# Performance work log

Hardware: AMD Instinct MI355X
Metric: run time of the kernel (lower is better)

The kernel has to match this reference:

```python
import jax, jax.numpy as jnp
import numpy as np

B, M, L, LQ, E, V = 32, 100, 30, 30, 256, 32000


def position_encoding(seq_len, emb):
    # faithful to MemN2N position encoding: 1 + 4*(k - (E+1)/2)*(j - (J+1)/2)/(E*J)
    j = jnp.arange(1, seq_len + 1, dtype=jnp.float32)[:, None]   # (J,1)
    k = jnp.arange(1, emb + 1, dtype=jnp.float32)[None, :]       # (1,E)
    half_e = (emb + 1) / 2.0
    half_j = (seq_len + 1) / 2.0
    return 1.0 + 4.0 * (k - half_e) * (j - half_j) / (emb * seq_len)  # (J,E)


def masked_softmax(x, m):
    xm = jnp.where(m > 0, x, -1e30)
    e = jnp.exp(xm - jnp.max(xm, axis=-1, keepdims=True)) * m
    return e / (jnp.sum(e, axis=-1, keepdims=True) + 1e-13)


def masked_log_softmax(x, m):
    return jax.nn.log_softmax(x + jnp.log(m + 1e-13), axis=-1)


def _forward(trainS, trainQ, trainVM, trainPM, trainSM, trainQM,
             A1, A2, A3, A4, W, b, gamma, beta):
    # query encoding: embed + position encode + query mask + sum over words
    Q = trainQ[:, 0, :]                                   # (B,LQ)
    pe_q = position_encoding(LQ, E)                       # (LQ,E)
    u = jnp.sum(A1[Q] * pe_q * trainQM[:, :, None], axis=1)  # (B,E)

    # story memory embeddings: gather + PE + sum over words.
    # NOTE: original code multiplies by trainSM but discards the result (bug),
    # so SM is intentionally NOT applied here.
    pe_s = position_encoding(L, E)                        # (L,E)
    embA1 = jnp.sum(A1[trainS] * pe_s, axis=2)            # (B,M,E)
    embA2 = jnp.sum(A2[trainS] * pe_s, axis=2)
    embA3 = jnp.sum(A3[trainS] * pe_s, axis=2)
    embA4 = jnp.sum(A4[trainS] * pe_s, axis=2)

    def hop(memA, memC, u):
        # scores = sum_E(memA * u) * PM (PM applied pre-sum is equivalent)
        scores = jnp.einsum('bme,be->bm', memA, u) * trainPM
        p = masked_softmax(scores, trainPM)               # (B,M)
        o = jnp.einsum('bm,bme->be', p, memC)             # (B,E)
        return o + u

    u = hop(embA1, embA2, u)   # hop 1
    u = hop(embA2, embA3, u)   # hop 2
    u = hop(embA3, embA4, u)   # hop 3

    # final linear + BatchNorm1d (training-mode batch stats, eps=1e-5)
    wx = u @ W.T + b                                      # (B,V)
    mean = jnp.mean(wx, axis=0)
    var = jnp.mean((wx - mean) ** 2, axis=0)
    y = gamma * (wx - mean) / jnp.sqrt(var + 1e-5) + beta
    return masked_log_softmax(y, trainVM)


def setup_inputs() -> dict:
    key = jax.random.key(0)
    ks = jax.random.split(key, 8)
    inp = {
        'trainS': jax.random.randint(ks[0], (B, M, L), 0, V, dtype=jnp.int32),
        'trainQ': jax.random.randint(ks[1], (B, 1, LQ), 0, V, dtype=jnp.int32),
        'trainVM': jnp.ones((B, V), jnp.float32),
        'trainPM': jnp.ones((B, M), jnp.float32),
        'trainSM': jnp.ones((B, M, L), jnp.float32),
        'trainQM': jnp.ones((B, LQ), jnp.float32),
        'A1': 0.1 * jax.random.normal(ks[2], (V, E), jnp.float32),
        'A2': 0.1 * jax.random.normal(ks[3], (V, E), jnp.float32),
        'A3': 0.1 * jax.random.normal(ks[4], (V, E), jnp.float32),
        'A4': 0.1 * jax.random.normal(ks[5], (V, E), jnp.float32),
        'W': jax.random.normal(ks[6], (V, E), jnp.float32) / np.sqrt(E),
        'b': jnp.zeros((V,), jnp.float32),
        'gamma': jnp.ones((V,), jnp.float32),
        'beta': jnp.zeros((V,), jnp.float32),
        'inspect': 0,
    }
    return inp


def reference(trainS, trainQ, trainVM, trainPM, trainSM, trainQM,
              A1, A2, A3, A4, W, b, gamma, beta, inspect):
    return _forward(trainS, trainQ, trainVM, trainPM, trainSM, trainQM,
                    A1, A2, A3, A4, W, b, gamma, beta)
```

## Files before the change

### kernel.cpp

```cpp
#include <hip/hip_runtime.h>
#include <math.h>

static constexpr int B_ = 32, M_ = 100, L_ = 30, LQ_ = 30, E_ = 256, V_ = 32000;

__global__ __launch_bounds__(256) void k_embed(const int* __restrict__ trainS,
                                               const float* __restrict__ A1,
                                               const float* __restrict__ A2,
                                               const float* __restrict__ A3,
                                               const float* __restrict__ A4,
                                               float* __restrict__ embA) {
    const int bm = blockIdx.x;
    const int tbl = threadIdx.x >> 6;
    const int e0 = (threadIdx.x & 63) * 4;
    const float* __restrict__ A = (tbl == 0) ? A1 : (tbl == 1) ? A2 : (tbl == 2) ? A3 : A4;
    const float half_e = (E_ + 1) * 0.5f;
    const float half_j = (L_ + 1) * 0.5f;
    const float inv = 1.0f / (float)(E_ * L_);
    const float k0 = (float)(e0 + 1) - half_e;
    const float k1 = k0 + 1.f, k2 = k0 + 2.f, k3 = k0 + 3.f;

    int idx[L_];
#pragma unroll
    for (int l = 0; l < L_; ++l) idx[l] = trainS[bm * L_ + l];

    float4 acc = make_float4(0.f, 0.f, 0.f, 0.f);
#pragma unroll
    for (int c = 0; c < 2; ++c) {
        float4 r[15];
#pragma unroll
        for (int j = 0; j < 15; ++j)
            r[j] = *reinterpret_cast<const float4*>(A + (size_t)idx[c * 15 + j] * E_ + e0);
        __builtin_amdgcn_sched_barrier(0);
#pragma unroll
        for (int j = 0; j < 15; ++j) {
            const int l = c * 15 + j;
            const float coef = 4.0f * ((float)(l + 1) - half_j) * inv;
            acc.x += r[j].x * (1.0f + coef * k0);
            acc.y += r[j].y * (1.0f + coef * k1);
            acc.z += r[j].z * (1.0f + coef * k2);
            acc.w += r[j].w * (1.0f + coef * k3);
        }
    }
    *reinterpret_cast<float4*>(embA + (size_t)tbl * (B_ * M_ * E_) + (size_t)bm * E_ + e0) = acc;
}

__global__ __launch_bounds__(1024) void k_hops(const int* __restrict__ trainQ,
                                               const float* __restrict__ trainQM,
                                               const float* __restrict__ A1,
                                               const float* __restrict__ embA,
                                               const float* __restrict__ trainPM,
                                               float* __restrict__ u_T) {
    const int b = blockIdx.x;
    const int tid = threadIdx.x;
    const int lane = tid & 63;
    const int wave = tid >> 6;
    const int g = tid >> 8;
    const int e = tid & 255;
    __shared__ float u_sh[E_];
    __shared__ float sc[M_];
    __shared__ float p_sh[M_];
    __shared__ float osum[4][E_];

    {
        const float half_e = (E_ + 1) * 0.5f;
        const float half_j = (LQ_ + 1) * 0.5f;
        const float inv = 1.0f / (float)(E_ * LQ_);
        const float ke = (float)(e + 1) - half_e;
        const int l0 = g * 8;
        const int ln = (LQ_ - l0 < 8) ? (LQ_ - l0) : 8;
        int qi[8];
        float qm[8];
#pragma unroll
        for (int j = 0; j < 8; ++j) {
            if (j < ln) {
                qi[j] = trainQ[b * LQ_ + l0 + j];
                qm[j] = trainQM[b * LQ_ + l0 + j];
            } else { qi[j] = 0; qm[j] = 0.f; }
        }
        float r[8];
#pragma unroll
        for (int j = 0; j < 8; ++j)
            r[j] = (j < ln) ? A1[(size_t)qi[j] * E_ + e] : 0.f;
        float part = 0.f;
#pragma unroll
        for (int j = 0; j < 8; ++j) {
            const float pe = 1.0f + 4.0f * ke * ((float)(l0 + j + 1) - half_j) * inv;
            part += r[j] * pe * qm[j];
        }
        osum[g][e] = part;
    }
    __syncthreads();
    if (tid < E_) u_sh[tid] = osum[0][tid] + osum[1][tid] + osum[2][tid] + osum[3][tid];
    __syncthreads();

    for (int hop = 0; hop < 3; ++hop) {
        const float* memA = embA + (size_t)hop * (B_ * M_ * E_) + (size_t)b * M_ * E_;
        const float* memC = memA + (size_t)(B_ * M_ * E_);
#pragma unroll 2
        for (int m = wave; m < M_; m += 16) {
            const float* row = memA + m * E_;
            float part = 0.f;
#pragma unroll
            for (int j = 0; j < 4; ++j)
                part += row[lane + 64 * j] * u_sh[lane + 64 * j];
#pragma unroll
            for (int off = 32; off > 0; off >>= 1)
                part += __shfl_xor(part, off, 64);
            if (lane == 0) sc[m] = part * trainPM[b * M_ + m];
        }
        __syncthreads();
        if (wave == 0) {
            const float pm0 = (lane < M_) ? trainPM[b * M_ + lane] : 0.f;
            const float pm1 = (lane + 64 < M_) ? trainPM[b * M_ + lane + 64] : 0.f;
            const float x0 = (lane < M_ && pm0 > 0.f) ? sc[lane] : -1e30f;
            const float x1 = (lane + 64 < M_ && pm1 > 0.f) ? sc[lane + 64] : -1e30f;
            float mx = fmaxf(x0, x1);
#pragma unroll
            for (int off = 32; off > 0; off >>= 1)
                mx = fmaxf(mx, __shfl_xor(mx, off, 64));
            const float e0v = (lane < M_) ? expf(x0 - mx) * pm0 : 0.f;
            const float e1v = (lane + 64 < M_) ? expf(x1 - mx) * pm1 : 0.f;
            float ssum = e0v + e1v;
#pragma unroll
            for (int off = 32; off > 0; off >>= 1)
                ssum += __shfl_xor(ssum, off, 64);
            const float invs = 1.0f / (ssum + 1e-13f);
            if (lane < M_) p_sh[lane] = e0v * invs;
            if (lane + 64 < M_) p_sh[lane + 64] = e1v * invs;
        }
        __syncthreads();
        {
            float acc = 0.f;
            const float* crow = memC + e;
            const int m0 = g * 25;
#pragma unroll 5
            for (int mm = 0; mm < 25; ++mm)
                acc += p_sh[m0 + mm] * crow[(size_t)(m0 + mm) * E_];
            osum[g][e] = acc;
        }
        __syncthreads();
        if (tid < E_) u_sh[tid] += osum[0][tid] + osum[1][tid] + osum[2][tid] + osum[3][tid];
        __syncthreads();
    }
    if (tid < E_) u_T[tid * B_ + b] = u_sh[tid];
}

__global__ __launch_bounds__(256) void k_output(const float* __restrict__ u_T,
                                                const float* __restrict__ Wm,
                                                const float* __restrict__ bias,
                                                const float* __restrict__ gamma,
                                                const float* __restrict__ beta,
                                                const float* __restrict__ VM,
                                                float* __restrict__ z) {
    __shared__ float u_lds[E_ * B_];
    const int tid = threadIdx.x;
    for (int i = tid; i < (E_ * B_) / 4; i += 256)
        reinterpret_cast<float4*>(u_lds)[i] = reinterpret_cast<const float4*>(u_T)[i];
    __syncthreads();

    const int bg = tid & 7;
    const int vl = tid >> 3;
    const int v0 = blockIdx.x * 64 + vl * 2;
    const int v1 = v0 + 1;
    const float* __restrict__ wr0 = Wm + (size_t)v0 * E_;
    const float* __restrict__ wr1 = Wm + (size_t)v1 * E_;

    float accA[4] = {0.f, 0.f, 0.f, 0.f};
    float accB[4] = {0.f, 0.f, 0.f, 0.f};

#pragma unroll
    for (int c = 0; c < 8; ++c) {
        float4 wa[8], wb[8];
#pragma unroll
        for (int j = 0; j < 8; ++j) {
            wa[j] = reinterpret_cast<const float4*>(wr0)[c * 8 + j];
            wb[j] = reinterpret_cast<const float4*>(wr1)[c * 8 + j];
        }
        __builtin_amdgcn_sched_barrier(0);
#pragma unroll
        for (int j = 0; j < 8; ++j) {
#pragma unroll
            for (int eo = 0; eo < 4; ++eo) {
                const int e = c * 32 + j * 4 + eo;
                const float4 u4 = *reinterpret_cast<const float4*>(u_lds + e * B_ + bg * 4);
                const float w0 = (eo == 0) ? wa[j].x : (eo == 1) ? wa[j].y : (eo == 2) ? wa[j].z : wa[j].w;
                const float w1 = (eo == 0) ? wb[j].x : (eo == 1) ? wb[j].y : (eo == 2) ? wb[j].z : wb[j].w;
                accA[0] += w0 * u4.x; accA[1] += w0 * u4.y; accA[2] += w0 * u4.z; accA[3] += w0 * u4.w;
                accB[0] += w1 * u4.x; accB[1] += w1 * u4.y; accB[2] += w1 * u4.z; accB[3] += w1 * u4.w;
            }
        }
    }

    const float bvA = bias[v0], bvB = bias[v1];
    float s1a = 0.f, s2a = 0.f, s1b = 0.f, s2b = 0.f;
#pragma unroll
    for (int i = 0; i < 4; ++i) {
        accA[i] += bvA; accB[i] += bvB;
        s1a += accA[i]; s2a += accA[i] * accA[i];
        s1b += accB[i]; s2b += accB[i] * accB[i];
    }
#pragma unroll
    for (int off = 1; off < 8; off <<= 1) {
        s1a += __shfl_xor(s1a, off, 64);
        s2a += __shfl_xor(s2a, off, 64);
        s1b += __shfl_xor(s1b, off, 64);
        s2b += __shfl_xor(s2b, off, 64);
    }
    const float meanA = s1a * (1.0f / B_);
    const float meanB = s1b * (1.0f / B_);
    const float varA = s2a * (1.0f / B_) - meanA * meanA;
    const float varB = s2b * (1.0f / B_) - meanB * meanB;
    const float rstdA = rsqrtf(varA + 1e-5f);
    const float rstdB = rsqrtf(varB + 1e-5f);
    const float gA = gamma[v0], beA = beta[v0];
    const float gB = gamma[v1], beB = beta[v1];

#pragma unroll
    for (int i = 0; i < 4; ++i) {
        const int b = bg * 4 + i;
        const size_t row = (size_t)b * V_;
        z[row + v0] = gA * (accA[i] - meanA) * rstdA + beA + logf(VM[row + v0] + 1e-13f);
        z[row + v1] = gB * (accB[i] - meanB) * rstdB + beB + logf(VM[row + v1] + 1e-13f);
    }
}

__global__ __launch_bounds__(256) void k_lsep(const float* __restrict__ z,
                                              float* __restrict__ partial) {
    const int b = blockIdx.x >> 3;
    const int k = blockIdx.x & 7;
    const int tid = threadIdx.x;
    const float4* zr = reinterpret_cast<const float4*>(z + (size_t)b * V_ + k * 4000);
    float s = 0.f;
    for (int i = tid; i < 1000; i += 256) {
        const float4 x = zr[i];
        s += expf(x.x) + expf(x.y) + expf(x.z) + expf(x.w);
    }
#pragma unroll
    for (int off = 32; off > 0; off >>= 1)
        s += __shfl_xor(s, off, 64);
    __shared__ float ss[4];
    const int wave = tid >> 6, lane = tid & 63;
    if (lane == 0) ss[wave] = s;
    __syncthreads();
    if (tid == 0) partial[blockIdx.x] = ss[0] + ss[1] + ss[2] + ss[3];
}

__global__ __launch_bounds__(256) void k_final(const float* __restrict__ z,
                                               const float* __restrict__ partial,
                                               float* __restrict__ out) {
    const int idx = blockIdx.x * 256 + threadIdx.x;
    const int b = idx / (V_ / 4);
    const int v4 = idx % (V_ / 4);
    float s = 0.f;
#pragma unroll
    for (int k = 0; k < 8; ++k) s += partial[b * 8 + k];
    const float lse = logf(s);
    const float4 x = reinterpret_cast<const float4*>(z + (size_t)b * V_)[v4];
    float4 o;
    o.x = x.x - lse; o.y = x.y - lse; o.z = x.z - lse; o.w = x.w - lse;
    reinterpret_cast<float4*>(out + (size_t)b * V_)[v4] = o;
}

extern "C" void kernel_launch(void* const* d_in, const int* in_sizes, int n_in,
                              void* d_out, int out_size, void* d_ws, size_t ws_size,
                              hipStream_t stream) {
    const int* trainS = (const int*)d_in[0];
    const int* trainQ = (const int*)d_in[1];
    const float* trainVM = (const float*)d_in[2];
    const float* trainPM = (const float*)d_in[3];
    const float* trainQM = (const float*)d_in[5];
    const float* A1 = (const float*)d_in[6];
    const float* A2 = (const float*)d_in[7];
    const float* A3 = (const float*)d_in[8];
    const float* A4 = (const float*)d_in[9];
    const float* Wm = (const float*)d_in[10];
    const float* bias = (const float*)d_in[11];
    const float* gamma = (const float*)d_in[12];
    const float* beta = (const float*)d_in[13];
    float* out = (float*)d_out;

    float* ws = (float*)d_ws;
    float* u_T = ws;
    float* embA = ws + 8192;
    float* z = embA + 4 * (B_ * M_ * E_);
    float* partial = z + (size_t)B_ * V_;

    k_embed<<<B_ * M_, 256, 0, stream>>>(trainS, A1, A2, A3, A4, embA);
    k_hops<<<B_, 1024, 0, stream>>>(trainQ, trainQM, A1, embA, trainPM, u_T);
    k_output<<<V_ / 64, 256, 0, stream>>>(u_T, Wm, bias, gamma, beta, trainVM, z);
    k_lsep<<<B_ * 8, 256, 0, stream>>>(z, partial);
    k_final<<<(B_ * V_ / 4) / 256, 256, 0, stream>>>(z, partial, out);
}
```

Baseline: 110.8 us.

## Fuse log-sum-exp partials into output kernel and regrid embedding gather

The separate k_lsep pass over z is removed. k_output now computes exp sums per batch row, reduces them in LDS, and atomically adds them into a per-row partial that k_hops zeroes beforehand. The logits are not max-shifted, which matches the old code. Separately, k_embed is regridded so each block handles one table and a 32-row slice of the embedding dimension, with token indices staged in shared memory. The aim is to cut one launch and a full read of z and to improve gather locality, at the cost of global atomics and a different load pattern.

```diff
diff --git a/kernel.cpp b/kernel.cpp
--- a/kernel.cpp
+++ b/kernel.cpp
@@ -9,31 +9,47 @@
                                                const float* __restrict__ A3,
                                                const float* __restrict__ A4,
                                                float* __restrict__ embA) {
-    const int bm = blockIdx.x;
-    const int tbl = threadIdx.x >> 6;
-    const int e0 = (threadIdx.x & 63) * 4;
-    const float* __restrict__ A = (tbl == 0) ? A1 : (tbl == 1) ? A2 : (tbl == 2) ? A3 : A4;
+    const int blk = blockIdx.x;
+    const int s = blk & 7;
+    const int q = blk >> 3;
+    const int t = q / 100;
+    const int i = q % 100;
+    const int tid = threadIdx.x;
+    const int w = tid >> 6;
+    const int lane = tid & 63;
+    const int g = lane >> 3;
+    const int sub = lane & 7;
+
+    const float* __restrict__ At = (t == 0) ? A1 : (t == 1) ? A2 : (t == 2) ? A3 : A4;
+
+    __shared__ int sidx[32 * L_];
+    for (int j = tid; j < 240; j += 256)
+        reinterpret_cast<int4*>(sidx)[j] = reinterpret_cast<const int4*>(trainS + i * 960)[j];
+    __syncthreads();
+
+    const int bm = i * 32 + w * 8 + g;
+    const int eoff = s * 32 + sub * 4;
     const float half_e = (E_ + 1) * 0.5f;
     const float half_j = (L_ + 1) * 0.5f;
     const float inv = 1.0f / (float)(E_ * L_);
-    const float k0 = (float)(e0 + 1) - half_e;
+    const float k0 = (float)(eoff + 1) - half_e;
     const float k1 = k0 + 1.f, k2 = k0 + 2.f, k3 = k0 + 3.f;
-
-    int idx[L_];
-#pragma unroll
-    for (int l = 0; l < L_; ++l) idx[l] = trainS[bm * L_ + l];
+    const int lbase = (w * 8 + g) * L_;
 
     float4 acc = make_float4(0.f, 0.f, 0.f, 0.f);
 #pragma unroll
-    for (int c = 0; c < 2; ++c) {
-        float4 r[15];
-#pragma unroll
-        for (int j = 0; j < 15; ++j)
-            r[j] = *reinterpret_cast<const float4*>(A + (size_t)idx[c * 15 + j] * E_ + e0);
+    for (int c = 0; c < 3; ++c) {
+        int id[10];
+#pragma unroll
+        for (int j = 0; j < 10; ++j) id[j] = sidx[lbase + c * 10 + j];
+        float4 r[10];
+#pragma unroll
+        for (int j = 0; j < 10; ++j)
+            r[j] = *reinterpret_cast<const float4*>(At + (size_t)id[j] * E_ + eoff);
         __builtin_amdgcn_sched_barrier(0);
 #pragma unroll
-        for (int j = 0; j < 15; ++j) {
-            const int l = c * 15 + j;
+        for (int j = 0; j < 10; ++j) {
+            const int l = c * 10 + j;
             const float coef = 4.0f * ((float)(l + 1) - half_j) * inv;
             acc.x += r[j].x * (1.0f + coef * k0);
             acc.y += r[j].y * (1.0f + coef * k1);
@@ -41,7 +57,7 @@
             acc.w += r[j].w * (1.0f + coef * k3);
         }
     }
-    *reinterpret_cast<float4*>(embA + (size_t)tbl * (B_ * M_ * E_) + (size_t)bm * E_ + e0) = acc;
+    *reinterpret_cast<float4*>(embA + (size_t)t * (B_ * M_ * E_) + (size_t)bm * E_ + eoff) = acc;
 }
 
 __global__ __launch_bounds__(1024) void k_hops(const int* __restrict__ trainQ,
@@ -49,13 +65,15 @@
                                                const float* __restrict__ A1,
                                                const float* __restrict__ embA,
                                                const float* __restrict__ trainPM,
-                                               float* __restrict__ u_T) {
+                                               float* __restrict__ u_T,
+                                               float* __restrict__ partial) {
     const int b = blockIdx.x;
     const int tid = threadIdx.x;
     const int lane = tid & 63;
     const int wave = tid >> 6;
     const int g = tid >> 8;
     const int e = tid & 255;
+    if (tid == 0) partial[b] = 0.f;
     __shared__ float u_sh[E_];
     __shared__ float sc[M_];
     __shared__ float p_sh[M_];
@@ -151,11 +169,14 @@
                                                 const float* __restrict__ gamma,
                                                 const float* __restrict__ beta,
                                                 const float* __restrict__ VM,
-                                                float* __restrict__ z) {
+                                                float* __restrict__ z,
+                                                float* __restrict__ partial) {
     __shared__ float u_lds[E_ * B_];
+    __shared__ float pex[B_];
     const int tid = threadIdx.x;
     for (int i = tid; i < (E_ * B_) / 4; i += 256)
         reinterpret_cast<float4*>(u_lds)[i] = reinterpret_cast<const float4*>(u_T)[i];
+    if (tid < B_) pex[tid] = 0.f;
     __syncthreads();
 
     const int bg = tid & 7;
@@ -215,34 +236,24 @@
     const float gA = gamma[v0], beA = beta[v0];
     const float gB = gamma[v1], beB = beta[v1];
 
+    float exs[4];
 #pragma unroll
     for (int i = 0; i < 4; ++i) {
         const int b = bg * 4 + i;
         const size_t row = (size_t)b * V_;
-        z[row + v0] = gA * (accA[i] - meanA) * rstdA + beA + logf(VM[row + v0] + 1e-13f);
-        z[row + v1] = gB * (accB[i] - meanB) * rstdB + beB + logf(VM[row + v1] + 1e-13f);
-    }
-}
-
-__global__ __launch_bounds__(256) void k_lsep(const float* __restrict__ z,
-                                              float* __restrict__ partial) {
-    const int b = blockIdx.x >> 3;
-    const int k = blockIdx.x & 7;
-    const int tid = threadIdx.x;
-    const float4* zr = reinterpret_cast<const float4*>(z + (size_t)b * V_ + k * 4000);
-    float s = 0.f;
-    for (int i = tid; i < 1000; i += 256) {
-        const float4 x = zr[i];
-        s += expf(x.x) + expf(x.y) + expf(x.z) + expf(x.w);
-    }
-#pragma unroll
-    for (int off = 32; off > 0; off >>= 1)
-        s += __shfl_xor(s, off, 64);
-    __shared__ float ss[4];
-    const int wave = tid >> 6, lane = tid & 63;
-    if (lane == 0) ss[wave] = s;
-    __syncthreads();
-    if (tid == 0) partial[blockIdx.x] = ss[0] + ss[1] + ss[2] + ss[3];
+        const float vm0 = VM[row + v0] + 1e-13f;
+        const float vm1 = VM[row + v1] + 1e-13f;
+        const float y0 = gA * (accA[i] - meanA) * rstdA + beA;
+        const float y1 = gB * (accB[i] - meanB) * rstdB + beB;
+        z[row + v0] = y0 + logf(vm0);
+        z[row + v1] = y1 + logf(vm1);
+        exs[i] = vm0 * expf(y0) + vm1 * expf(y1);
+    }
+#pragma unroll
+    for (int i = 0; i < 4; ++i)
+        atomicAdd(&pex[bg * 4 + i], exs[i]);
+    __syncthreads();
+    if (tid < B_) atomicAdd(&partial[tid], pex[tid]);
 }
 
 __global__ __launch_bounds__(256) void k_final(const float* __restrict__ z,
@@ -251,10 +262,7 @@
     const int idx = blockIdx.x * 256 + threadIdx.x;
     const int b = idx / (V_ / 4);
     const int v4 = idx % (V_ / 4);
-    float s = 0.f;
-#pragma unroll
-    for (int k = 0; k < 8; ++k) s += partial[b * 8 + k];
-    const float lse = logf(s);
+    const float lse = logf(partial[b]);
     const float4 x = reinterpret_cast<const float4*>(z + (size_t)b * V_)[v4];
     float4 o;
     o.x = x.x - lse; o.y = x.y - lse; o.z = x.z - lse; o.w = x.w - lse;
@@ -285,9 +293,8 @@
     float* z = embA + 4 * (B_ * M_ * E_);
     float* partial = z + (size_t)B_ * V_;
 
-    k_embed<<<B_ * M_, 256, 0, stream>>>(trainS, A1, A2, A3, A4, embA);
-    k_hops<<<B_, 1024, 0, stream>>>(trainQ, trainQM, A1, embA, trainPM, u_T);
-    k_output<<<V_ / 64, 256, 0, stream>>>(u_T, Wm, bias, gamma, beta, trainVM, z);
-    k_lsep<<<B_ * 8, 256, 0, stream>>>(z, partial);
+    k_embed<<<B_ * M_ * 4, 256, 0, stream>>>(trainS, A1, A2, A3, A4, embA);
+    k_hops<<<B_, 1024, 0, stream>>>(trainQ, trainQM, A1, embA, trainPM, u_T, partial);
+    k_output<<<V_ / 64, 256, 0, stream>>>(u_T, Wm, bias, gamma, beta, trainVM, z, partial);
     k_final<<<(B_ * V_ / 4) / 256, 256, 0, stream>>>(z, partial, out);
 }
```

After: 153.3 us. +38.3%, slower.
